# Kernel tuning notes

Measured on AMD Instinct MI355X. Metric: run time of the kernel, lower is better.

## Reference

```python
import jax, jax.numpy as jnp
import numpy as np

N, NOBJ, M, H, W = 512, 16, 8192, 128, 128


def _rand_rotations(key, n):
    A = jax.random.normal(key, (n, 3, 3), dtype=jnp.float32)
    q, r = jnp.linalg.qr(A)
    q = q * jnp.sign(jnp.diagonal(r, axis1=-2, axis2=-1))[:, None, :]
    det = jnp.linalg.det(q)  # +-1; flip first column if det == -1
    q = q.at[:, :, 0].multiply(det[:, None])
    return q


def setup_inputs() -> dict:
    key = jax.random.key(0)
    ks = jax.random.split(key, 10)
    obj_id = jax.random.randint(ks[0], (N,), 0, NOBJ, dtype=jnp.int32)
    # realistic pinhole intrinsics (pixels), slight per-sample jitter
    base_K = jnp.array([[600.0, 0.0, 64.0], [0.0, 600.0, 64.0], [0.0, 0.0, 1.0]], jnp.float32)
    cam_K = base_K[None] + jax.random.normal(ks[1], (N, 3, 3)) * jnp.array(
        [[5.0, 0.0, 1.0], [0.0, 5.0, 1.0], [0.0, 0.0, 0.0]], jnp.float32)
    gt_R = _rand_rotations(ks[2], N)
    # small rotational perturbation for pred
    pred_R = _rand_rotations(ks[3], N) @ gt_R
    gt_t = jnp.concatenate([jax.random.normal(ks[4], (N, 2)) * 20.0,
                            500.0 + jax.random.uniform(ks[4], (N, 1)) * 300.0], axis=-1)
    pred_t = gt_t + jax.random.normal(ks[5], (N, 3)) * 5.0
    mesh_points = jax.random.normal(ks[6], (NOBJ, M, 3)) * 50.0  # mm-scale meshes
    diameters = 150.0 + jax.random.uniform(ks[7], (NOBJ,)) * 150.0
    gt_coord_3d_roi = jax.random.normal(ks[8], (N, 3, H, W)) * 50.0
    gt_mask_vis_roi = jax.random.bernoulli(ks[9], 0.4, (N, 1, H, W))
    return dict(obj_id=obj_id, cam_K=cam_K, gt_cam_R_m2c=gt_R, gt_cam_t_m2c=gt_t,
                pred_cam_R_m2c=pred_R, pred_cam_t_m2c=pred_t,
                gt_coord_3d_roi=gt_coord_3d_roi, gt_mask_vis_roi=gt_mask_vis_roi,
                mesh_points=mesh_points, diameters=diameters)


def _project(K, x):
    # K: [N,3,3], x: [N,...,3] -> pixel coords [N,...,2]
    h = jnp.einsum('nij,n...j->n...i', K, x)
    return h[..., :2] / h[..., 2:3]


def reference(obj_id, cam_K, gt_cam_R_m2c, gt_cam_t_m2c, pred_cam_R_m2c,
              pred_cam_t_m2c, gt_coord_3d_roi, gt_mask_vis_roi, mesh_points, diameters):
    # RE (degrees)
    R_diff = pred_cam_R_m2c @ jnp.swapaxes(gt_cam_R_m2c, -2, -1)
    trace = R_diff[..., 0, 0] + R_diff[..., 1, 1] + R_diff[..., 2, 2]
    re = jnp.arccos((jnp.clip(trace, -1.0, 3.0) - 1.0) * 0.5) * (180.0 / jnp.pi)
    # TE (cm)
    te = jnp.linalg.norm(pred_cam_t_m2c - gt_cam_t_m2c, axis=-1) * 100.0
    # ADD: mean distance between transformed mesh points, / diameter
    pts = mesh_points[obj_id]                      # [N,M,3]
    dR = pred_cam_R_m2c - gt_cam_R_m2c
    dt = pred_cam_t_m2c - gt_cam_t_m2c
    diff = jnp.einsum('nij,nmj->nmi', dR, pts) + dt[:, None, :]
    ad = jnp.linalg.norm(diff, axis=-1).mean(axis=-1) / diameters[obj_id]
    # PROJ: mean projected distance over mesh points
    xp = jnp.einsum('nij,nmj->nmi', pred_cam_R_m2c, pts) + pred_cam_t_m2c[:, None, :]
    xg = jnp.einsum('nij,nmj->nmi', gt_cam_R_m2c, pts) + gt_cam_t_m2c[:, None, :]
    pj = jnp.linalg.norm(_project(cam_K, xp) - _project(cam_K, xg), axis=-1).mean(axis=-1)
    # PROJ-visible: same over visible ROI pixels (masked mean instead of ragged gather)
    verts = jnp.transpose(gt_coord_3d_roi, (0, 2, 3, 1))  # [N,H,W,3]
    vp = jnp.einsum('nij,nhwj->nhwi', pred_cam_R_m2c, verts) + pred_cam_t_m2c[:, None, None, :]
    vg = jnp.einsum('nij,nhwj->nhwi', gt_cam_R_m2c, verts) + gt_cam_t_m2c[:, None, None, :]
    d = jnp.linalg.norm(_project(cam_K, vp) - _project(cam_K, vg), axis=-1)  # [N,H,W]
    mask = gt_mask_vis_roi[:, 0].astype(d.dtype)
    pv = (d * mask).sum(axis=(1, 2)) / jnp.maximum(mask.sum(axis=(1, 2)), 1.0)
    return re, te, ad, pj, pv
```

## Files before the change

kernel.cpp:

```cpp
#include <hip/hip_runtime.h>
#include <math.h>

#define NS    512
#define NOBJ  16
#define MPTS  8192
#define HH    128
#define WW    128
#define HW    (HH * WW)
#define BLOCK 256
#define SPLIT 4
#define NWAVE (BLOCK / 64)
#define P2_IT (HW / 4 / SPLIT / BLOCK)
#define P1_IT (MPTS / SPLIT / (BLOCK * 4))

__device__ __forceinline__ float frcp(float x)  { return __builtin_amdgcn_rcpf(x); }
__device__ __forceinline__ float fsqrt(float x) { return __builtin_amdgcn_sqrtf(x); }
__device__ __forceinline__ float rfl(float x) {
    return __int_as_float(__builtin_amdgcn_readfirstlane(__float_as_int(x)));
}

__global__ __launch_bounds__(BLOCK, 4) void score_partial(
    const int*   __restrict__ obj_id,
    const float* __restrict__ cam_K,
    const float* __restrict__ gt_R,
    const float* __restrict__ gt_t,
    const float* __restrict__ pr_R,
    const float* __restrict__ pr_t,
    const float* __restrict__ coord,
    const int*   __restrict__ mask,
    const float* __restrict__ mesh,
    float*       __restrict__ ws,
    float*       __restrict__ out)
{
    const int b   = blockIdx.x;
    const int n   = b >> 2;
    const int c   = b & (SPLIT - 1);
    const int tid = threadIdx.x;

    const float* cx = coord + (size_t)n * 3 * HW;
    const float4* cx4 = (const float4*)cx;
    const float4* cy4 = (const float4*)(cx + HW);
    const float4* cz4 = (const float4*)(cx + 2 * HW);
    const int4*   mk4 = (const int4*)(mask + (size_t)n * HW);

    float4 AX[P2_IT], AY[P2_IT], AZ[P2_IT];
    int4   AM[P2_IT];
#pragma unroll
    for (int it = 0; it < P2_IT; ++it) {
        const int p = c * (HW / 4 / SPLIT) + it * BLOCK + tid;
        AX[it] = cx4[p];
        AY[it] = cy4[p];
        AZ[it] = cz4[p];
        AM[it] = mk4[p];
    }

    const int obj = __builtin_amdgcn_readfirstlane(obj_id[n]);
    const float4* mp4 = (const float4*)(mesh + (size_t)obj * MPTS * 3);
    float4 MF[P1_IT][3];
#pragma unroll
    for (int it = 0; it < P1_IT; ++it) {
        const int k = c * (MPTS / SPLIT / 4) + it * BLOCK + tid;
        MF[it][0] = mp4[k * 3 + 0];
        MF[it][1] = mp4[k * 3 + 1];
        MF[it][2] = mp4[k * 3 + 2];
    }

    float K[9], Rg[9], Rp[9], tg[3], tp[3];
#pragma unroll
    for (int i = 0; i < 9; ++i) {
        K[i]  = cam_K[n * 9 + i];
        Rg[i] = gt_R [n * 9 + i];
        Rp[i] = pr_R [n * 9 + i];
    }
#pragma unroll
    for (int i = 0; i < 3; ++i) {
        tg[i] = gt_t[n * 3 + i];
        tp[i] = pr_t[n * 3 + i];
    }

    if (c == 0 && tid == 0) {
        float trace = 0.0f;
#pragma unroll
        for (int i = 0; i < 9; ++i) trace += Rp[i] * Rg[i];
        trace = fminf(fmaxf(trace, -1.0f), 3.0f);
        out[0 * NS + n] = acosf((trace - 1.0f) * 0.5f) * (180.0f / 3.14159265358979323846f);
        const float dx = tp[0] - tg[0], dy = tp[1] - tg[1], dz = tp[2] - tg[2];
        out[1 * NS + n] = sqrtf(dx * dx + dy * dy + dz * dz) * 100.0f;
    }

    float dR[9], dt[3], Ap[9], Ag[9], bp[3], bg[3];
#pragma unroll
    for (int i = 0; i < 9; ++i) dR[i] = rfl(Rp[i] - Rg[i]);
#pragma unroll
    for (int i = 0; i < 3; ++i) dt[i] = rfl(tp[i] - tg[i]);
#pragma unroll
    for (int r = 0; r < 3; ++r) {
#pragma unroll
        for (int col = 0; col < 3; ++col) {
            Ap[r * 3 + col] = rfl(K[r * 3 + 0] * Rp[0 * 3 + col]
                                + K[r * 3 + 1] * Rp[1 * 3 + col]
                                + K[r * 3 + 2] * Rp[2 * 3 + col]);
            Ag[r * 3 + col] = rfl(K[r * 3 + 0] * Rg[0 * 3 + col]
                                + K[r * 3 + 1] * Rg[1 * 3 + col]
                                + K[r * 3 + 2] * Rg[2 * 3 + col]);
        }
        bp[r] = rfl(K[r * 3 + 0] * tp[0] + K[r * 3 + 1] * tp[1] + K[r * 3 + 2] * tp[2]);
        bg[r] = rfl(K[r * 3 + 0] * tg[0] + K[r * 3 + 1] * tg[1] + K[r * 3 + 2] * tg[2]);
    }

    float s_ad = 0.0f, s_pj = 0.0f;
#pragma unroll
    for (int it = 0; it < P1_IT; ++it) {
        const float4 f0 = MF[it][0], f1 = MF[it][1], f2 = MF[it][2];
        const float px[4] = {f0.x, f0.w, f1.z, f2.y};
        const float py[4] = {f0.y, f1.x, f1.w, f2.z};
        const float pz[4] = {f0.z, f1.y, f2.x, f2.w};
#pragma unroll
        for (int j = 0; j < 4; ++j) {
            const float x = px[j], y = py[j], z = pz[j];
            const float dx = fmaf(dR[0], x, fmaf(dR[1], y, fmaf(dR[2], z, dt[0])));
            const float dy = fmaf(dR[3], x, fmaf(dR[4], y, fmaf(dR[5], z, dt[1])));
            const float dz = fmaf(dR[6], x, fmaf(dR[7], y, fmaf(dR[8], z, dt[2])));
            s_ad += fsqrt(fmaf(dx, dx, fmaf(dy, dy, dz * dz)));
            const float hpx = fmaf(Ap[0], x, fmaf(Ap[1], y, fmaf(Ap[2], z, bp[0])));
            const float hpy = fmaf(Ap[3], x, fmaf(Ap[4], y, fmaf(Ap[5], z, bp[1])));
            const float hpz = fmaf(Ap[6], x, fmaf(Ap[7], y, fmaf(Ap[8], z, bp[2])));
            const float hgx = fmaf(Ag[0], x, fmaf(Ag[1], y, fmaf(Ag[2], z, bg[0])));
            const float hgy = fmaf(Ag[3], x, fmaf(Ag[4], y, fmaf(Ag[5], z, bg[1])));
            const float hgz = fmaf(Ag[6], x, fmaf(Ag[7], y, fmaf(Ag[8], z, bg[2])));
            const float iwp = frcp(hpz), iwg = frcp(hgz);
            const float du = fmaf(hpx, iwp, -hgx * iwg);
            const float dv = fmaf(hpy, iwp, -hgy * iwg);
            s_pj += fsqrt(fmaf(du, du, dv * dv));
        }
    }

    float s_pv = 0.0f, s_m = 0.0f;
#pragma unroll
    for (int it = 0; it < P2_IT; ++it) {
        const float xs[4] = {AX[it].x, AX[it].y, AX[it].z, AX[it].w};
        const float ys[4] = {AY[it].x, AY[it].y, AY[it].z, AY[it].w};
        const float zs[4] = {AZ[it].x, AZ[it].y, AZ[it].z, AZ[it].w};
        const int   ms[4] = {AM[it].x, AM[it].y, AM[it].z, AM[it].w};
#pragma unroll
        for (int j = 0; j < 4; ++j) {
            const float x = xs[j], y = ys[j], z = zs[j];
            const float hpx = fmaf(Ap[0], x, fmaf(Ap[1], y, fmaf(Ap[2], z, bp[0])));
            const float hpy = fmaf(Ap[3], x, fmaf(Ap[4], y, fmaf(Ap[5], z, bp[1])));
            const float hpz = fmaf(Ap[6], x, fmaf(Ap[7], y, fmaf(Ap[8], z, bp[2])));
            const float hgx = fmaf(Ag[0], x, fmaf(Ag[1], y, fmaf(Ag[2], z, bg[0])));
            const float hgy = fmaf(Ag[3], x, fmaf(Ag[4], y, fmaf(Ag[5], z, bg[1])));
            const float hgz = fmaf(Ag[6], x, fmaf(Ag[7], y, fmaf(Ag[8], z, bg[2])));
            const float iwp = frcp(hpz), iwg = frcp(hgz);
            const float du = fmaf(hpx, iwp, -hgx * iwg);
            const float dv = fmaf(hpy, iwp, -hgy * iwg);
            const float d  = fsqrt(fmaf(du, du, dv * dv));
            const float fm = (ms[j] != 0) ? 1.0f : 0.0f;
            s_pv += d * fm;
            s_m  += fm;
        }
    }

    float vals[4] = {s_ad, s_pj, s_pv, s_m};
#pragma unroll
    for (int k = 0; k < 4; ++k) {
#pragma unroll
        for (int off = 32; off > 0; off >>= 1)
            vals[k] += __shfl_down(vals[k], off, 64);
    }
    __shared__ float red[4][NWAVE];
    const int wave = tid >> 6;
    const int lane = tid & 63;
    if (lane == 0) {
#pragma unroll
        for (int k = 0; k < 4; ++k) red[k][wave] = vals[k];
    }
    __syncthreads();
    if (tid == 0) {
#pragma unroll
        for (int k = 0; k < 4; ++k) {
            float s = 0.0f;
#pragma unroll
            for (int w = 0; w < NWAVE; ++w) s += red[k][w];
            ws[(size_t)(n * SPLIT + c) * 4 + k] = s;
        }
    }
}

__global__ __launch_bounds__(256) void score_reduce(
    const float* __restrict__ ws,
    const int*   __restrict__ obj_id,
    const float* __restrict__ diam,
    float*       __restrict__ out)
{
    const int n = blockIdx.x * blockDim.x + threadIdx.x;
    if (n >= NS) return;
    float ad = 0.0f, pj = 0.0f, pv = 0.0f, m = 0.0f;
#pragma unroll
    for (int cb = 0; cb < SPLIT; ++cb) {
        const float* p = ws + (size_t)(n * SPLIT + cb) * 4;
        ad += p[0]; pj += p[1]; pv += p[2]; m += p[3];
    }
    const float dia = diam[obj_id[n]];
    out[2 * NS + n] = ad * (1.0f / MPTS) / dia;
    out[3 * NS + n] = pj * (1.0f / MPTS);
    out[4 * NS + n] = pv / fmaxf(m, 1.0f);
}

extern "C" void kernel_launch(void* const* d_in, const int* in_sizes, int n_in,
                              void* d_out, int out_size, void* d_ws, size_t ws_size,
                              hipStream_t stream) {
    const int*   obj_id = (const int*)  d_in[0];
    const float* cam_K  = (const float*)d_in[1];
    const float* gt_R   = (const float*)d_in[2];
    const float* gt_t   = (const float*)d_in[3];
    const float* pr_R   = (const float*)d_in[4];
    const float* pr_t   = (const float*)d_in[5];
    const float* coord  = (const float*)d_in[6];
    const int*   mask   = (const int*)  d_in[7];
    const float* mesh   = (const float*)d_in[8];
    const float* diam   = (const float*)d_in[9];
    float* out = (float*)d_out;
    float* ws  = (float*)d_ws;

    score_partial<<<NS * SPLIT, BLOCK, 0, stream>>>(obj_id, cam_K, gt_R, gt_t, pr_R,
                                                    pr_t, coord, mask, mesh, ws, out);
    score_reduce<<<(NS + 255) / 256, 256, 0, stream>>>(ws, obj_id, diam, out);
}
```

Before: 189.8 us.

## Split fused kernel into separate pixel and mesh kernels with finer pixel split

Splits the single fused partial kernel into a pixel-visibility kernel (8 blocks per sample) and a mesh kernel (4 blocks per sample). RE/TE are now computed in the reduce kernel instead of one thread of the partial kernel. Each kernel holds fewer registers and the pixel work is spread over more blocks, which is meant to raise occupancy and parallelism on the memory-bound pixel pass. The cost is an extra kernel launch and serialization between the two passes on the same stream.

Result: slower. 198.6 us (+4.6%).

```diff
diff --git a/kernel.cpp b/kernel.cpp
--- a/kernel.cpp
+++ b/kernel.cpp
@@ -1,17 +1,18 @@
 #include <hip/hip_runtime.h>
 #include <math.h>
 
-#define NS    512
-#define NOBJ  16
-#define MPTS  8192
-#define HH    128
-#define WW    128
-#define HW    (HH * WW)
-#define BLOCK 256
-#define SPLIT 4
-#define NWAVE (BLOCK / 64)
-#define P2_IT (HW / 4 / SPLIT / BLOCK)
-#define P1_IT (MPTS / SPLIT / (BLOCK * 4))
+#define NS     512
+#define NOBJ   16
+#define MPTS   8192
+#define HH     128
+#define WW     128
+#define HW     (HH * WW)
+#define BLOCK  256
+#define PSPLIT 8
+#define MSPLIT 4
+#define P_IT   (HW / 4 / PSPLIT / BLOCK)
+#define M_IT   (MPTS / MSPLIT / (BLOCK * 4))
+#define NWAVE  (BLOCK / 64)
 
 __device__ __forceinline__ float frcp(float x)  { return __builtin_amdgcn_rcpf(x); }
 __device__ __forceinline__ float fsqrt(float x) { return __builtin_amdgcn_sqrtf(x); }
@@ -19,8 +20,27 @@
     return __int_as_float(__builtin_amdgcn_readfirstlane(__float_as_int(x)));
 }
 
-__global__ __launch_bounds__(BLOCK, 4) void score_partial(
-    const int*   __restrict__ obj_id,
+__device__ __forceinline__ void fuse_proj(const float* __restrict__ cam_K,
+                                          const float* __restrict__ R,
+                                          const float* __restrict__ t, int n,
+                                          float A[9], float b[3]) {
+    float K[9], Rr[9], tt[3];
+#pragma unroll
+    for (int i = 0; i < 9; ++i) { K[i] = cam_K[n * 9 + i]; Rr[i] = R[n * 9 + i]; }
+#pragma unroll
+    for (int i = 0; i < 3; ++i) tt[i] = t[n * 3 + i];
+#pragma unroll
+    for (int r = 0; r < 3; ++r) {
+#pragma unroll
+        for (int c = 0; c < 3; ++c)
+            A[r * 3 + c] = rfl(K[r * 3 + 0] * Rr[0 * 3 + c]
+                             + K[r * 3 + 1] * Rr[1 * 3 + c]
+                             + K[r * 3 + 2] * Rr[2 * 3 + c]);
+        b[r] = rfl(K[r * 3 + 0] * tt[0] + K[r * 3 + 1] * tt[1] + K[r * 3 + 2] * tt[2]);
+    }
+}
+
+__global__ __launch_bounds__(BLOCK) void score_pixels(
     const float* __restrict__ cam_K,
     const float* __restrict__ gt_R,
     const float* __restrict__ gt_t,
@@ -28,13 +48,11 @@
     const float* __restrict__ pr_t,
     const float* __restrict__ coord,
     const int*   __restrict__ mask,
-    const float* __restrict__ mesh,
-    float*       __restrict__ ws,
-    float*       __restrict__ out)
+    float*       __restrict__ wsB)
 {
     const int b   = blockIdx.x;
-    const int n   = b >> 2;
-    const int c   = b & (SPLIT - 1);
+    const int n   = b >> 3;
+    const int c   = b & (PSPLIT - 1);
     const int tid = threadIdx.x;
 
     const float* cx = coord + (size_t)n * 3 * HW;
@@ -43,74 +61,106 @@
     const float4* cz4 = (const float4*)(cx + 2 * HW);
     const int4*   mk4 = (const int4*)(mask + (size_t)n * HW);
 
-    float4 AX[P2_IT], AY[P2_IT], AZ[P2_IT];
-    int4   AM[P2_IT];
-#pragma unroll
-    for (int it = 0; it < P2_IT; ++it) {
-        const int p = c * (HW / 4 / SPLIT) + it * BLOCK + tid;
+    float4 AX[P_IT], AY[P_IT], AZ[P_IT];
+    int4   AM[P_IT];
+#pragma unroll
+    for (int it = 0; it < P_IT; ++it) {
+        const int p = c * (HW / 4 / PSPLIT) + it * BLOCK + tid;
         AX[it] = cx4[p];
         AY[it] = cy4[p];
         AZ[it] = cz4[p];
         AM[it] = mk4[p];
     }
 
+    float Ap[9], Ag[9], bp[3], bg[3];
+    fuse_proj(cam_K, pr_R, pr_t, n, Ap, bp);
+    fuse_proj(cam_K, gt_R, gt_t, n, Ag, bg);
+
+    float s_pv = 0.0f, s_m = 0.0f;
+#pragma unroll
+    for (int it = 0; it < P_IT; ++it) {
+        const float xs[4] = {AX[it].x, AX[it].y, AX[it].z, AX[it].w};
+        const float ys[4] = {AY[it].x, AY[it].y, AY[it].z, AY[it].w};
+        const float zs[4] = {AZ[it].x, AZ[it].y, AZ[it].z, AZ[it].w};
+        const int   ms[4] = {AM[it].x, AM[it].y, AM[it].z, AM[it].w};
+#pragma unroll
+        for (int j = 0; j < 4; ++j) {
+            const float x = xs[j], y = ys[j], z = zs[j];
+            const float hpx = fmaf(Ap[0], x, fmaf(Ap[1], y, fmaf(Ap[2], z, bp[0])));
+            const float hpy = fmaf(Ap[3], x, fmaf(Ap[4], y, fmaf(Ap[5], z, bp[1])));
+            const float hpz = fmaf(Ap[6], x, fmaf(Ap[7], y, fmaf(Ap[8], z, bp[2])));
+            const float hgx = fmaf(Ag[0], x, fmaf(Ag[1], y, fmaf(Ag[2], z, bg[0])));
+            const float hgy = fmaf(Ag[3], x, fmaf(Ag[4], y, fmaf(Ag[5], z, bg[1])));
+            const float hgz = fmaf(Ag[6], x, fmaf(Ag[7], y, fmaf(Ag[8], z, bg[2])));
+            const float iwp = frcp(hpz), iwg = frcp(hgz);
+            const float du = fmaf(hpx, iwp, -hgx * iwg);
+            const float dv = fmaf(hpy, iwp, -hgy * iwg);
+            const float d  = fsqrt(fmaf(du, du, dv * dv));
+            const float fm = (ms[j] != 0) ? 1.0f : 0.0f;
+            s_pv += d * fm;
+            s_m  += fm;
+        }
+    }
+
+    float vals[2] = {s_pv, s_m};
+#pragma unroll
+    for (int k = 0; k < 2; ++k)
+#pragma unroll
+        for (int off = 32; off > 0; off >>= 1)
+            vals[k] += __shfl_down(vals[k], off, 64);
+
+    __shared__ float red[2][NWAVE];
+    const int wave = tid >> 6, lane = tid & 63;
+    if (lane == 0) { red[0][wave] = vals[0]; red[1][wave] = vals[1]; }
+    __syncthreads();
+    if (tid == 0) {
+        float pv = 0.0f, m = 0.0f;
+#pragma unroll
+        for (int w = 0; w < NWAVE; ++w) { pv += red[0][w]; m += red[1][w]; }
+        wsB[(size_t)(n * PSPLIT + c) * 2 + 0] = pv;
+        wsB[(size_t)(n * PSPLIT + c) * 2 + 1] = m;
+    }
+}
+
+__global__ __launch_bounds__(BLOCK) void score_mesh(
+    const int*   __restrict__ obj_id,
+    const float* __restrict__ cam_K,
+    const float* __restrict__ gt_R,
+    const float* __restrict__ gt_t,
+    const float* __restrict__ pr_R,
+    const float* __restrict__ pr_t,
+    const float* __restrict__ mesh,
+    float*       __restrict__ wsA)
+{
+    const int b   = blockIdx.x;
+    const int n   = b >> 2;
+    const int c   = b & (MSPLIT - 1);
+    const int tid = threadIdx.x;
+
     const int obj = __builtin_amdgcn_readfirstlane(obj_id[n]);
     const float4* mp4 = (const float4*)(mesh + (size_t)obj * MPTS * 3);
-    float4 MF[P1_IT][3];
-#pragma unroll
-    for (int it = 0; it < P1_IT; ++it) {
-        const int k = c * (MPTS / SPLIT / 4) + it * BLOCK + tid;
+
+    float4 MF[M_IT][3];
+#pragma unroll
+    for (int it = 0; it < M_IT; ++it) {
+        const int k = c * (MPTS / MSPLIT / 4) + it * BLOCK + tid;
         MF[it][0] = mp4[k * 3 + 0];
         MF[it][1] = mp4[k * 3 + 1];
         MF[it][2] = mp4[k * 3 + 2];
     }
 
-    float K[9], Rg[9], Rp[9], tg[3], tp[3];
-#pragma unroll
-    for (int i = 0; i < 9; ++i) {
-        K[i]  = cam_K[n * 9 + i];
-        Rg[i] = gt_R [n * 9 + i];
-        Rp[i] = pr_R [n * 9 + i];
-    }
-#pragma unroll
-    for (int i = 0; i < 3; ++i) {
-        tg[i] = gt_t[n * 3 + i];
-        tp[i] = pr_t[n * 3 + i];
-    }
-
-    if (c == 0 && tid == 0) {
-        float trace = 0.0f;
-#pragma unroll
-        for (int i = 0; i < 9; ++i) trace += Rp[i] * Rg[i];
-        trace = fminf(fmaxf(trace, -1.0f), 3.0f);
-        out[0 * NS + n] = acosf((trace - 1.0f) * 0.5f) * (180.0f / 3.14159265358979323846f);
-        const float dx = tp[0] - tg[0], dy = tp[1] - tg[1], dz = tp[2] - tg[2];
-        out[1 * NS + n] = sqrtf(dx * dx + dy * dy + dz * dz) * 100.0f;
-    }
-
-    float dR[9], dt[3], Ap[9], Ag[9], bp[3], bg[3];
-#pragma unroll
-    for (int i = 0; i < 9; ++i) dR[i] = rfl(Rp[i] - Rg[i]);
-#pragma unroll
-    for (int i = 0; i < 3; ++i) dt[i] = rfl(tp[i] - tg[i]);
-#pragma unroll
-    for (int r = 0; r < 3; ++r) {
-#pragma unroll
-        for (int col = 0; col < 3; ++col) {
-            Ap[r * 3 + col] = rfl(K[r * 3 + 0] * Rp[0 * 3 + col]
-                                + K[r * 3 + 1] * Rp[1 * 3 + col]
-                                + K[r * 3 + 2] * Rp[2 * 3 + col]);
-            Ag[r * 3 + col] = rfl(K[r * 3 + 0] * Rg[0 * 3 + col]
-                                + K[r * 3 + 1] * Rg[1 * 3 + col]
-                                + K[r * 3 + 2] * Rg[2 * 3 + col]);
-        }
-        bp[r] = rfl(K[r * 3 + 0] * tp[0] + K[r * 3 + 1] * tp[1] + K[r * 3 + 2] * tp[2]);
-        bg[r] = rfl(K[r * 3 + 0] * tg[0] + K[r * 3 + 1] * tg[1] + K[r * 3 + 2] * tg[2]);
-    }
+    float Ap[9], Ag[9], bp[3], bg[3];
+    fuse_proj(cam_K, pr_R, pr_t, n, Ap, bp);
+    fuse_proj(cam_K, gt_R, gt_t, n, Ag, bg);
+    float dR[9], dt[3];
+#pragma unroll
+    for (int i = 0; i < 9; ++i) dR[i] = rfl(pr_R[n * 9 + i] - gt_R[n * 9 + i]);
+#pragma unroll
+    for (int i = 0; i < 3; ++i) dt[i] = rfl(pr_t[n * 3 + i] - gt_t[n * 3 + i]);
 
     float s_ad = 0.0f, s_pj = 0.0f;
 #pragma unroll
-    for (int it = 0; it < P1_IT; ++it) {
+    for (int it = 0; it < M_IT; ++it) {
         const float4 f0 = MF[it][0], f1 = MF[it][1], f2 = MF[it][2];
         const float px[4] = {f0.x, f0.w, f1.z, f2.y};
         const float py[4] = {f0.y, f1.x, f1.w, f2.z};
@@ -135,73 +185,64 @@
         }
     }
 
-    float s_pv = 0.0f, s_m = 0.0f;
-#pragma unroll
-    for (int it = 0; it < P2_IT; ++it) {
-        const float xs[4] = {AX[it].x, AX[it].y, AX[it].z, AX[it].w};
-        const float ys[4] = {AY[it].x, AY[it].y, AY[it].z, AY[it].w};
-        const float zs[4] = {AZ[it].x, AZ[it].y, AZ[it].z, AZ[it].w};
-        const int   ms[4] = {AM[it].x, AM[it].y, AM[it].z, AM[it].w};
-#pragma unroll
-        for (int j = 0; j < 4; ++j) {
-            const float x = xs[j], y = ys[j], z = zs[j];
-            const float hpx = fmaf(Ap[0], x, fmaf(Ap[1], y, fmaf(Ap[2], z, bp[0])));
-            const float hpy = fmaf(Ap[3], x, fmaf(Ap[4], y, fmaf(Ap[5], z, bp[1])));
-            const float hpz = fmaf(Ap[6], x, fmaf(Ap[7], y, fmaf(Ap[8], z, bp[2])));
-            const float hgx = fmaf(Ag[0], x, fmaf(Ag[1], y, fmaf(Ag[2], z, bg[0])));
-            const float hgy = fmaf(Ag[3], x, fmaf(Ag[4], y, fmaf(Ag[5], z, bg[1])));
-            const float hgz = fmaf(Ag[6], x, fmaf(Ag[7], y, fmaf(Ag[8], z, bg[2])));
-            const float iwp = frcp(hpz), iwg = frcp(hgz);
-            const float du = fmaf(hpx, iwp, -hgx * iwg);
-            const float dv = fmaf(hpy, iwp, -hgy * iwg);
-            const float d  = fsqrt(fmaf(du, du, dv * dv));
-            const float fm = (ms[j] != 0) ? 1.0f : 0.0f;
-            s_pv += d * fm;
-            s_m  += fm;
-        }
-    }
-
-    float vals[4] = {s_ad, s_pj, s_pv, s_m};
-#pragma unroll
-    for (int k = 0; k < 4; ++k) {
+    float vals[2] = {s_ad, s_pj};
+#pragma unroll
+    for (int k = 0; k < 2; ++k)
 #pragma unroll
         for (int off = 32; off > 0; off >>= 1)
             vals[k] += __shfl_down(vals[k], off, 64);
-    }
-    __shared__ float red[4][NWAVE];
-    const int wave = tid >> 6;
-    const int lane = tid & 63;
-    if (lane == 0) {
-#pragma unroll
-        for (int k = 0; k < 4; ++k) red[k][wave] = vals[k];
-    }
+
+    __shared__ float red[2][NWAVE];
+    const int wave = tid >> 6, lane = tid & 63;
+    if (lane == 0) { red[0][wave] = vals[0]; red[1][wave] = vals[1]; }
     __syncthreads();
     if (tid == 0) {
-#pragma unroll
-        for (int k = 0; k < 4; ++k) {
-            float s = 0.0f;
-#pragma unroll
-            for (int w = 0; w < NWAVE; ++w) s += red[k][w];
-            ws[(size_t)(n * SPLIT + c) * 4 + k] = s;
-        }
+        float ad = 0.0f, pj = 0.0f;
+#pragma unroll
+        for (int w = 0; w < NWAVE; ++w) { ad += red[0][w]; pj += red[1][w]; }
+        wsA[(size_t)(n * MSPLIT + c) * 2 + 0] = ad;
+        wsA[(size_t)(n * MSPLIT + c) * 2 + 1] = pj;
     }
 }
 
 __global__ __launch_bounds__(256) void score_reduce(
-    const float* __restrict__ ws,
+    const float* __restrict__ wsA,
+    const float* __restrict__ wsB,
     const int*   __restrict__ obj_id,
+    const float* __restrict__ gt_R,
+    const float* __restrict__ gt_t,
+    const float* __restrict__ pr_R,
+    const float* __restrict__ pr_t,
     const float* __restrict__ diam,
     float*       __restrict__ out)
 {
     const int n = blockIdx.x * blockDim.x + threadIdx.x;
     if (n >= NS) return;
-    float ad = 0.0f, pj = 0.0f, pv = 0.0f, m = 0.0f;
-#pragma unroll
-    for (int cb = 0; cb < SPLIT; ++cb) {
-        const float* p = ws + (size_t)(n * SPLIT + cb) * 4;
-        ad += p[0]; pj += p[1]; pv += p[2]; m += p[3];
-    }
+
+    float ad = 0.0f, pj = 0.0f;
+#pragma unroll
+    for (int cb = 0; cb < MSPLIT; ++cb) {
+        ad += wsA[(size_t)(n * MSPLIT + cb) * 2 + 0];
+        pj += wsA[(size_t)(n * MSPLIT + cb) * 2 + 1];
+    }
+    float pv = 0.0f, m = 0.0f;
+#pragma unroll
+    for (int cb = 0; cb < PSPLIT; ++cb) {
+        pv += wsB[(size_t)(n * PSPLIT + cb) * 2 + 0];
+        m  += wsB[(size_t)(n * PSPLIT + cb) * 2 + 1];
+    }
+
+    float trace = 0.0f;
+#pragma unroll
+    for (int i = 0; i < 9; ++i) trace += pr_R[n * 9 + i] * gt_R[n * 9 + i];
+    trace = fminf(fmaxf(trace, -1.0f), 3.0f);
+    const float dx = pr_t[n * 3 + 0] - gt_t[n * 3 + 0];
+    const float dy = pr_t[n * 3 + 1] - gt_t[n * 3 + 1];
+    const float dz = pr_t[n * 3 + 2] - gt_t[n * 3 + 2];
+
     const float dia = diam[obj_id[n]];
+    out[0 * NS + n] = acosf((trace - 1.0f) * 0.5f) * (180.0f / 3.14159265358979323846f);
+    out[1 * NS + n] = sqrtf(dx * dx + dy * dy + dz * dz) * 100.0f;
     out[2 * NS + n] = ad * (1.0f / MPTS) / dia;
     out[3 * NS + n] = pj * (1.0f / MPTS);
     out[4 * NS + n] = pv / fmaxf(m, 1.0f);
@@ -221,9 +262,13 @@
     const float* mesh   = (const float*)d_in[8];
     const float* diam   = (const float*)d_in[9];
     float* out = (float*)d_out;
-    float* ws  = (float*)d_ws;
-
-    score_partial<<<NS * SPLIT, BLOCK, 0, stream>>>(obj_id, cam_K, gt_R, gt_t, pr_R,
-                                                    pr_t, coord, mask, mesh, ws, out);
-    score_reduce<<<(NS + 255) / 256, 256, 0, stream>>>(ws, obj_id, diam, out);
-}
+    float* wsA = (float*)d_ws;
+    float* wsB = wsA + (size_t)NS * MSPLIT * 2;
+
+    score_pixels<<<NS * PSPLIT, BLOCK, 0, stream>>>(cam_K, gt_R, gt_t, pr_R, pr_t,
+                                                    coord, mask, wsB);
+    score_mesh<<<NS * MSPLIT, BLOCK, 0, stream>>>(obj_id, cam_K, gt_R, gt_t, pr_R,
+                                                  pr_t, mesh, wsA);
+    score_reduce<<<(NS + 255) / 256, 256, 0, stream>>>(wsA, wsB, obj_id, gt_R, gt_t,
+                                                       pr_R, pr_t, diam, out);
+}
```
